# Optimization experiments

Measured on AMD Instinct MI355X. Metric: run time of the kernel, lower is better.

The kernel has to match this reference:

```python
import jax, jax.numpy as jnp
import numpy as np


def setup_inputs() -> dict:
    key = jax.random.key(0)
    ks = jax.random.split(key, 11)
    B, S, D, K = 8, 2048, 512, 256
    s = lambda k, shp, fan: jax.random.normal(k, shp, dtype=jnp.float32) / np.sqrt(fan)
    return {
        "x": jax.random.normal(ks[0], (B, S, D), dtype=jnp.float32),
        "Wk1": s(ks[1], (D, K), D), "bk1": jnp.zeros((K,), jnp.float32),
        "Wq1": s(ks[2], (D, K), D), "bq1": jnp.zeros((K,), jnp.float32),
        "Wk2": s(ks[3], (D, K), D), "bk2": jnp.zeros((K,), jnp.float32),
        "Wq2": s(ks[4], (D, K), D), "bq2": jnp.zeros((K,), jnp.float32),
        "Wv2": s(ks[5], (D, D), D), "bv2": jnp.zeros((D,), jnp.float32),
    }


def _attn(q, k, v):
    # raw scores with NO 1/sqrt(d) scaling, softmax over key axis, then AV
    scores = jax.nn.softmax(jnp.einsum('bqd,bkd->bqk', q, k), axis=-1)
    return jnp.einsum('bqk,bkd->bqd', scores, v)


def _block2(h, Wk2, bk2, Wq2, bq2, Wv2, bv2):
    k = h @ Wk2 + bk2
    q = h @ Wq2 + bq2
    v = h @ Wv2 + bv2
    v = v / jnp.linalg.norm(v, axis=2, keepdims=True)  # L2-normalize values
    return _attn(q, k, v)


def reference(x, Wk1, bk1, Wq1, bq1, Wk2, bk2, Wq2, bq2, Wv2, bv2):
    # block 1: values are the raw input x
    k1 = x @ Wk1 + bk1
    q1 = x @ Wq1 + bq1
    outputs = _attn(q1, k1, x)
    # blocks 2 and 3 reuse the SAME layer-2 weights (as in the torch forward)
    hidden = _block2(outputs, Wk2, bk2, Wq2, bq2, Wv2, bv2)
    final = _block2(hidden, Wk2, bk2, Wq2, bq2, Wv2, bv2)
    return final[0, -1, :]
```

## Files before the change

kernel.cpp:

```cpp
#include <hip/hip_runtime.h>
#include <math.h>

typedef __attribute__((ext_vector_type(8))) short short8;
typedef __attribute__((ext_vector_type(4))) float f32x4;

__device__ inline unsigned short f2bf_rn(float f) {
    unsigned u = __builtin_bit_cast(unsigned, f);
    u += 0x7FFF + ((u >> 16) & 1);
    return (unsigned short)(u >> 16);
}
__device__ inline float bf2f(unsigned short h) {
    unsigned u = ((unsigned)h) << 16;
    return __builtin_bit_cast(float, u);
}

#define ISSUE(ST, RA, RB)                                                      \
  do {                                                                         \
    int s_ = (ST);                                                             \
    int sg_ = s_ / SPS;                                                        \
    int k0_ = (s_ - sg_ * SPS) * 64;                                           \
    const unsigned short* Ap_ = (sg_ < 2) ? Ah : Al;                           \
    const unsigned short* Bp_ = (sg_ == 1) ? Bl : Bh;                          \
    _Pragma("unroll") for (int i_ = 0; i_ < 4; ++i_) {                         \
      RA[i_] = *(const uint4*)(Ap_ + (size_t)(bm + crow[i_]) * lda + k0_ + csl[i_] * 8); \
      RB[i_] = *(const uint4*)(Bp_ + (size_t)(bn + crow[i_]) * ldb + k0_ + csl[i_] * 8); \
    }                                                                          \
  } while (0)

#define PHASE(IT, RWa, RWb, RLa, RLb)                                          \
  do {                                                                         \
    _Pragma("unroll") for (int i_ = 0; i_ < 4; ++i_) {                         \
      int wsl_ = csl[i_] ^ (crow[i_] & 7);                                     \
      *(uint4*)&As[crow[i_]][wsl_ * 8] = RWa[i_];                              \
      *(uint4*)&Bs[crow[i_]][wsl_ * 8] = RWb[i_];                              \
    }                                                                          \
    if ((IT) + 1 < CHUNK) { ISSUE(st0 + (IT) + 1, RLa, RLb); }                 \
    asm volatile("s_waitcnt lgkmcnt(0)\n\ts_barrier" ::: "memory");            \
    _Pragma("unroll") for (int kk = 0; kk < 2; ++kk) {                         \
      short8 af[4], bf[4];                                                     \
      _Pragma("unroll") for (int f = 0; f < 4; ++f) {                          \
        int ar = wm * 64 + f * 16 + r15;                                       \
        int as_ = (kk * 4 + ksl) ^ (ar & 7);                                   \
        af[f] = *(const short8*)&As[ar][as_ * 8];                              \
        int br = wn * 64 + f * 16 + r15;                                       \
        int bs_ = (kk * 4 + ksl) ^ (br & 7);                                   \
        bf[f] = *(const short8*)&Bs[br][bs_ * 8];                              \
      }                                                                        \
      _Pragma("unroll") for (int i_ = 0; i_ < 4; ++i_)                         \
        _Pragma("unroll") for (int j_ = 0; j_ < 4; ++j_)                       \
          acc[i_][j_] = __builtin_amdgcn_mfma_f32_16x16x32_bf16(               \
              af[i_], bf[j_], acc[i_][j_], 0, 0, 0);                           \
    }                                                                          \
    asm volatile("s_barrier" ::: "memory");                                    \
  } while (0)

template <int KSEG, int NSPLIT>
__global__ __launch_bounds__(256, 2) void gemm_bf16(
    const unsigned short* __restrict__ Ah, const unsigned short* __restrict__ Al, int lda,
    const unsigned short* __restrict__ Bh, const unsigned short* __restrict__ Bl, int ldb,
    float* __restrict__ Cout, int ldc)
{
    constexpr int SPS = KSEG / 64;
    constexpr int NST = 3 * SPS;
    constexpr int CHUNK = NST / NSPLIT;

    __shared__ __align__(16) unsigned short As[128][64];
    __shared__ __align__(16) unsigned short Bs[128][64];

    const int tid = threadIdx.x, lane = tid & 63, w = tid >> 6;
    const int wm = w >> 1, wn = w & 1;
    const int bm = blockIdx.y * 128, bn = blockIdx.x * 128;
    const int st0 = blockIdx.z * CHUNK;
    const int r15 = lane & 15, ksl = lane >> 4;

    int crow[4], csl[4];
#pragma unroll
    for (int i = 0; i < 4; ++i) { int c = tid + i * 256; crow[i] = c >> 3; csl[i] = c & 7; }

    f32x4 acc[4][4];
#pragma unroll
    for (int i = 0; i < 4; ++i)
#pragma unroll
        for (int j = 0; j < 4; ++j) acc[i][j] = (f32x4){0.f, 0.f, 0.f, 0.f};

    uint4 rA0[4], rB0[4], rA1[4], rB1[4];
    ISSUE(st0, rA0, rB0);

#pragma unroll 1
    for (int it = 0; it < CHUNK; it += 2) {
        PHASE(it,     rA0, rB0, rA1, rB1);
        PHASE(it + 1, rA1, rB1, rA0, rB0);
    }

    float* Cz = Cout + (size_t)blockIdx.z * (size_t)(gridDim.y * 128) * ldc;
#pragma unroll
    for (int i = 0; i < 4; ++i) {
        int rowb = bm + wm * 64 + i * 16 + (lane >> 4) * 4;
#pragma unroll
        for (int j = 0; j < 4; ++j) {
            int colb = bn + wn * 64 + j * 16 + r15;
#pragma unroll
            for (int r = 0; r < 4; ++r)
                Cz[(size_t)(rowb + r) * ldc + colb] = acc[i][j][r];
        }
    }
}

template <int NS, bool BIAS>
__global__ __launch_bounds__(256) void reduce_kernel(
    const float* __restrict__ part, size_t pstride4,
    const float* __restrict__ bias, float* __restrict__ C,
    unsigned short* __restrict__ Ch, unsigned short* __restrict__ Cl, int N)
{
    size_t idx = (size_t)blockIdx.x * 256 + threadIdx.x;
    const float4* p = (const float4*)part;
    float4 s = p[idx];
#pragma unroll
    for (int z = 1; z < NS; ++z) {
        float4 t = p[idx + (size_t)z * pstride4];
        s.x += t.x; s.y += t.y; s.z += t.z; s.w += t.w;
    }
    if (BIAS) {
        int col = (int)((idx * 4) & (size_t)(N - 1));
        s.x += bias[col]; s.y += bias[col + 1]; s.z += bias[col + 2]; s.w += bias[col + 3];
    }
    ((float4*)C)[idx] = s;
    float v[4] = {s.x, s.y, s.z, s.w};
    unsigned short h[4], l[4];
#pragma unroll
    for (int q = 0; q < 4; ++q) { h[q] = f2bf_rn(v[q]); l[q] = f2bf_rn(v[q] - bf2f(h[q])); }
    uint2 hp = make_uint2((unsigned)h[0] | ((unsigned)h[1] << 16), (unsigned)h[2] | ((unsigned)h[3] << 16));
    uint2 lp = make_uint2((unsigned)l[0] | ((unsigned)l[1] << 16), (unsigned)l[2] | ((unsigned)l[3] << 16));
    ((uint2*)Ch)[idx] = hp;
    ((uint2*)Cl)[idx] = lp;
}

__global__ __launch_bounds__(256) void softmax_ph(
    const float* __restrict__ Sc, unsigned short* __restrict__ Ph,
    unsigned short* __restrict__ Pl)
{
    __shared__ float red[8];
    const int tid = threadIdx.x;
    const size_t r = blockIdx.x;
    const float4* p4 = (const float4*)(Sc + r * 2048);
    float4 a = p4[tid * 2], b = p4[tid * 2 + 1];
    float vv[8] = {a.x, a.y, a.z, a.w, b.x, b.y, b.z, b.w};

    float mx = vv[0];
#pragma unroll
    for (int i = 1; i < 8; ++i) mx = fmaxf(mx, vv[i]);
#pragma unroll
    for (int o = 32; o; o >>= 1) mx = fmaxf(mx, __shfl_down(mx, o));
    if ((tid & 63) == 0) red[tid >> 6] = mx;
    __syncthreads();
    mx = fmaxf(fmaxf(red[0], red[1]), fmaxf(red[2], red[3]));

    float e[8], sum = 0.f;
#pragma unroll
    for (int i = 0; i < 8; ++i) { e[i] = expf(vv[i] - mx); sum += e[i]; }
#pragma unroll
    for (int o = 32; o; o >>= 1) sum += __shfl_down(sum, o);
    __syncthreads();
    if ((tid & 63) == 0) red[4 + (tid >> 6)] = sum;
    __syncthreads();
    float inv = 1.f / (red[4] + red[5] + red[6] + red[7]);

    unsigned short h[8], l[8];
#pragma unroll
    for (int i = 0; i < 8; ++i) {
        float pv = e[i] * inv;
        h[i] = f2bf_rn(pv);
        l[i] = f2bf_rn(pv - bf2f(h[i]));
    }
    uint4 hp, lp;
    hp.x = (unsigned)h[0] | ((unsigned)h[1] << 16); hp.y = (unsigned)h[2] | ((unsigned)h[3] << 16);
    hp.z = (unsigned)h[4] | ((unsigned)h[5] << 16); hp.w = (unsigned)h[6] | ((unsigned)h[7] << 16);
    lp.x = (unsigned)l[0] | ((unsigned)l[1] << 16); lp.y = (unsigned)l[2] | ((unsigned)l[3] << 16);
    lp.z = (unsigned)l[4] | ((unsigned)l[5] << 16); lp.w = (unsigned)l[6] | ((unsigned)l[7] << 16);
    ((uint4*)(Ph + r * 2048))[tid] = hp;
    ((uint4*)(Pl + r * 2048))[tid] = lp;
}

__global__ __launch_bounds__(256) void l2norm_kernel(float* __restrict__ V, int ld,
                                                     int coloff, int D)
{
    __shared__ float red[8];
    const int tid = threadIdx.x;
    float* p = V + (size_t)blockIdx.x * ld + coloff;
    float s = 0.f;
    for (int i = tid; i < D; i += 256) { float v = p[i]; s = fmaf(v, v, s); }
#pragma unroll
    for (int o = 32; o; o >>= 1) s += __shfl_down(s, o);
    if ((tid & 63) == 0) red[tid >> 6] = s;
    __syncthreads();
    float scale = 1.f / sqrtf(red[0] + red[1] + red[2] + red[3]);
    for (int i = tid; i < D; i += 256) p[i] *= scale;
}

__global__ __launch_bounds__(256) void tc_kernel(
    const float* __restrict__ in, int ldin,
    unsigned short* __restrict__ oh, unsigned short* __restrict__ ol,
    int ldo, int rowoff)
{
    __shared__ float tile[32][33];
    int bx = blockIdx.x * 32, by = blockIdx.y * 32;
    int tx = threadIdx.x & 31, ty = threadIdx.x >> 5;
#pragma unroll
    for (int i = 0; i < 32; i += 8)
        tile[ty + i][tx] = in[(size_t)(by + ty + i) * ldin + bx + tx];
    __syncthreads();
#pragma unroll
    for (int i = 0; i < 32; i += 8) {
        float v = tile[tx][ty + i];
        unsigned short h = f2bf_rn(v);
        unsigned short l = f2bf_rn(v - bf2f(h));
        size_t o = (size_t)(rowoff + bx + ty + i) * ldo + by + tx;
        oh[o] = h; ol[o] = l;
    }
}

__global__ __launch_bounds__(256) void convert_hl(
    const float* __restrict__ in, unsigned short* __restrict__ oh,
    unsigned short* __restrict__ ol)
{
    size_t idx = (size_t)blockIdx.x * 256 + threadIdx.x;
    float4 s = ((const float4*)in)[idx];
    float v[4] = {s.x, s.y, s.z, s.w};
    unsigned short h[4], l[4];
#pragma unroll
    for (int q = 0; q < 4; ++q) { h[q] = f2bf_rn(v[q]); l[q] = f2bf_rn(v[q] - bf2f(h[q])); }
    uint2 hp = make_uint2((unsigned)h[0] | ((unsigned)h[1] << 16), (unsigned)h[2] | ((unsigned)h[3] << 16));
    uint2 lp = make_uint2((unsigned)l[0] | ((unsigned)l[1] << 16), (unsigned)l[2] | ((unsigned)l[3] << 16));
    ((uint2*)oh)[idx] = hp;
    ((uint2*)ol)[idx] = lp;
}

__global__ __launch_bounds__(256) void concat_bias(
    const float* bk1, const float* bq1, const float* bk2, const float* bq2,
    const float* bv2, float* b1, float* b2)
{
    int i = blockIdx.x * 256 + threadIdx.x;
    if (i < 512) b1[i] = (i < 256) ? bk1[i] : bq1[i - 256];
    if (i < 1024) b2[i] = (i < 256) ? bk2[i] : (i < 512 ? bq2[i - 256] : bv2[i - 512]);
}

template <bool HAS_BIAS>
__global__ __launch_bounds__(256) void gemv_nt(
    const float* __restrict__ a, const float* __restrict__ Bt, int ldb,
    const float* __restrict__ bias, float* __restrict__ out, int K)
{
    int w = threadIdx.x >> 6, lane = threadIdx.x & 63;
    int n = blockIdx.x * 4 + w;
    const float* row = Bt + (size_t)n * ldb;
    float s = 0.f;
    for (int k = lane; k < K; k += 64) s = fmaf(a[k], row[k], s);
#pragma unroll
    for (int o = 32; o; o >>= 1) s += __shfl_down(s, o);
    if (lane == 0) out[n] = HAS_BIAS ? s + bias[n] : s;
}

__global__ __launch_bounds__(256) void gemv_hl(
    const float* __restrict__ p, const unsigned short* __restrict__ Vh,
    const unsigned short* __restrict__ Vl, int ld, float* __restrict__ out, int K)
{
    int w = threadIdx.x >> 6, lane = threadIdx.x & 63;
    int d = blockIdx.x * 4 + w;
    const unsigned short* rh = Vh + (size_t)d * ld;
    const unsigned short* rl = Vl + (size_t)d * ld;
    float s = 0.f;
    for (int k = lane; k < K; k += 64) s = fmaf(p[k], bf2f(rh[k]) + bf2f(rl[k]), s);
#pragma unroll
    for (int o = 32; o; o >>= 1) s += __shfl_down(s, o);
    if (lane == 0) out[d] = s;
}

__global__ __launch_bounds__(256) void softmax_f32(float* __restrict__ S, int L)
{
    __shared__ float row[2048];
    __shared__ float red[8];
    const int tid = threadIdx.x;
    float* p = S + (size_t)blockIdx.x * L;
    float mx = -1e30f;
    for (int i = tid; i < L; i += 256) { float v = p[i]; row[i] = v; mx = fmaxf(mx, v); }
#pragma unroll
    for (int o = 32; o; o >>= 1) mx = fmaxf(mx, __shfl_down(mx, o));
    if ((tid & 63) == 0) red[tid >> 6] = mx;
    __syncthreads();
    mx = fmaxf(fmaxf(red[0], red[1]), fmaxf(red[2], red[3]));
    float sum = 0.f;
    for (int i = tid; i < L; i += 256) { float e = expf(row[i] - mx); row[i] = e; sum += e; }
#pragma unroll
    for (int o = 32; o; o >>= 1) sum += __shfl_down(sum, o);
    __syncthreads();
    if ((tid & 63) == 0) red[4 + (tid >> 6)] = sum;
    __syncthreads();
    float inv = 1.f / (red[4] + red[5] + red[6] + red[7]);
    for (int i = tid; i < L; i += 256) p[i] = row[i] * inv;
}

extern "C" void kernel_launch(void* const* d_in, const int* in_sizes, int n_in,
                              void* d_out, int out_size, void* d_ws, size_t ws_size,
                              hipStream_t stream)
{
    const float* x   = (const float*)d_in[0];
    const float* Wk1 = (const float*)d_in[1];
    const float* bk1 = (const float*)d_in[2];
    const float* Wq1 = (const float*)d_in[3];
    const float* bq1 = (const float*)d_in[4];
    const float* Wk2 = (const float*)d_in[5];
    const float* bk2 = (const float*)d_in[6];
    const float* Wq2 = (const float*)d_in[7];
    const float* bq2 = (const float*)d_in[8];
    const float* Wv2 = (const float*)d_in[9];
    const float* bv2 = (const float*)d_in[10];
    float* out = (float*)d_out;

    const int S = 2048, D = 512;
    typedef unsigned short us;

    char* p = (char*)d_ws;
    float* C    = (float*)p;            p += (size_t)S * 1024 * 4;
    float* SCP  = (float*)p;            p += (size_t)S * S * 4;
    float* H    = (float*)p;            p += (size_t)S * D * 4;
    us* Ph  = (us*)p; p += (size_t)S * S * 2;
    us* Pl  = (us*)p; p += (size_t)S * S * 2;
    us* Chh = (us*)p; p += (size_t)S * 1024 * 2;
    us* Cll = (us*)p; p += (size_t)S * 1024 * 2;
    us* Hh  = (us*)p; p += (size_t)S * D * 2;
    us* Hl  = (us*)p; p += (size_t)S * D * 2;
    us* xh  = (us*)p; p += (size_t)S * D * 2;
    us* xl  = (us*)p; p += (size_t)S * D * 2;
    us* VTh = (us*)p; p += (size_t)D * S * 2;
    us* VTl = (us*)p; p += (size_t)D * S * 2;
    us* WT1h = (us*)p; p += (size_t)512 * 512 * 2;
    us* WT1l = (us*)p; p += (size_t)512 * 512 * 2;
    us* WT2h = (us*)p; p += (size_t)1024 * 512 * 2;
    us* WT2l = (us*)p; p += (size_t)1024 * 512 * 2;
    float* b1 = (float*)p; p += 512 * 4;
    float* b2 = (float*)p; p += 1024 * 4;

    dim3 blk(256);
    const size_t PSTR  = (size_t)S * 512 / 4;
    const size_t PSTR2 = (size_t)S * 1024 / 4;

    convert_hl<<<dim3(S * D / 1024), blk, 0, stream>>>(x, xh, xl);
    tc_kernel<<<dim3(16, 64), blk, 0, stream>>>(x, 512, VTh, VTl, S, 0);
    tc_kernel<<<dim3(8, 16), blk, 0, stream>>>(Wk1, 256, WT1h, WT1l, 512, 0);
    tc_kernel<<<dim3(8, 16), blk, 0, stream>>>(Wq1, 256, WT1h, WT1l, 512, 256);
    tc_kernel<<<dim3(8, 16), blk, 0, stream>>>(Wk2, 256, WT2h, WT2l, 512, 0);
    tc_kernel<<<dim3(8, 16), blk, 0, stream>>>(Wq2, 256, WT2h, WT2l, 512, 256);
    tc_kernel<<<dim3(16, 16), blk, 0, stream>>>(Wv2, 512, WT2h, WT2l, 512, 512);
    concat_bias<<<dim3(4), blk, 0, stream>>>(bk1, bq1, bk2, bq2, bv2, b1, b2);

    gemm_bf16<512, 3><<<dim3(4, 16, 3), blk, 0, stream>>>(xh, xl, 512, WT1h, WT1l, 512, SCP, 512);
    reduce_kernel<3, true><<<dim3(S * 512 / 1024), blk, 0, stream>>>(SCP, PSTR, b1, C, Chh, Cll, 512);
    gemm_bf16<256, 1><<<dim3(16, 16, 1), blk, 0, stream>>>(Chh + 256, Cll + 256, 512, Chh, Cll, 512, SCP, 2048);
    softmax_ph<<<dim3(S), blk, 0, stream>>>(SCP, Ph, Pl);
    gemm_bf16<2048, 4><<<dim3(4, 16, 4), blk, 0, stream>>>(Ph, Pl, 2048, VTh, VTl, 2048, SCP, 512);
    reduce_kernel<4, false><<<dim3(S * 512 / 1024), blk, 0, stream>>>(SCP, PSTR, nullptr, H, Hh, Hl, 512);

    gemm_bf16<512, 2><<<dim3(8, 16, 2), blk, 0, stream>>>(Hh, Hl, 512, WT2h, WT2l, 512, SCP, 1024);
    reduce_kernel<2, true><<<dim3(S * 1024 / 1024), blk, 0, stream>>>(SCP, PSTR2, b2, C, Chh, Cll, 1024);
    l2norm_kernel<<<dim3(S), blk, 0, stream>>>(C, 1024, 512, 512);
    tc_kernel<<<dim3(16, 64), blk, 0, stream>>>(C + 512, 1024, VTh, VTl, S, 0);
    gemm_bf16<256, 1><<<dim3(16, 16, 1), blk, 0, stream>>>(Chh + 256, Cll + 256, 1024, Chh, Cll, 1024, SCP, 2048);
    softmax_ph<<<dim3(S), blk, 0, stream>>>(SCP, Ph, Pl);
    gemm_bf16<2048, 4><<<dim3(4, 16, 4), blk, 0, stream>>>(Ph, Pl, 2048, VTh, VTl, 2048, SCP, 512);
    reduce_kernel<4, false><<<dim3(S * 512 / 1024), blk, 0, stream>>>(SCP, PSTR, nullptr, H, Hh, Hl, 512);

    gemm_bf16<512, 2><<<dim3(8, 16, 2), blk, 0, stream>>>(Hh, Hl, 512, WT2h, WT2l, 512, SCP, 1024);
    reduce_kernel<2, true><<<dim3(S * 1024 / 1024), blk, 0, stream>>>(SCP, PSTR2, b2, C, Chh, Cll, 1024);
    l2norm_kernel<<<dim3(S), blk, 0, stream>>>(C, 1024, 512, 512);
    tc_kernel<<<dim3(16, 64), blk, 0, stream>>>(C + 512, 1024, VTh, VTl, S, 0);
    gemv_nt<false><<<dim3(S / 4), blk, 0, stream>>>(C + (size_t)(S - 1) * 1024 + 256, C, 1024, nullptr, SCP, 256);
    softmax_f32<<<dim3(1), blk, 0, stream>>>(SCP, S);
    gemv_hl<<<dim3(D / 4), blk, 0, stream>>>(SCP, VTh, VTl, S, out, S);
}
```

Before: 476.9 us.

## Replace materialized score/softmax/PV pipeline with split-K flash attention and combine

The separate QK^T GEMM, row softmax, split-K PV GEMM and reduce are replaced by a fused flash-attention kernel. Each block handles 64 queries over a 256-key slice, keeps an online max and sum, and skips rescaling when the running max grows by no more than 8. A combine kernel then merges the eight key-split partials into hi/lo bf16 outputs. This avoids writing and reading the 2048x2048 fp32 score matrix and the bf16 probability matrices. In exchange it writes 8 fp32 output partials per query and uses a heavy register footprint with many barriers per tile.

```diff
diff --git a/kernel.cpp b/kernel.cpp
--- a/kernel.cpp
+++ b/kernel.cpp
@@ -3,6 +3,7 @@
 
 typedef __attribute__((ext_vector_type(8))) short short8;
 typedef __attribute__((ext_vector_type(4))) float f32x4;
+typedef unsigned short ushort_t;
 
 __device__ inline unsigned short f2bf_rn(float f) {
     unsigned u = __builtin_bit_cast(unsigned, f);
@@ -135,50 +136,216 @@
     ((uint2*)Cl)[idx] = lp;
 }
 
-__global__ __launch_bounds__(256) void softmax_ph(
-    const float* __restrict__ Sc, unsigned short* __restrict__ Ph,
-    unsigned short* __restrict__ Pl)
-{
-    __shared__ float red[8];
+#define SLK(r, s) ((s) ^ (((s) >> 3) & 3) ^ ((((r) ^ ((r) >> 3))) & 7))
+
+__global__ __launch_bounds__(256, 2) void flash_attn(
+    const unsigned short* __restrict__ Qh, const unsigned short* __restrict__ Ql,
+    const unsigned short* __restrict__ Kh, const unsigned short* __restrict__ Kl,
+    int ldqk,
+    const unsigned short* __restrict__ VTh, const unsigned short* __restrict__ VTl,
+    float* __restrict__ Opart, float* __restrict__ Mpart, float* __restrict__ Lpart)
+{
+    const int tid = threadIdx.x, lane = tid & 63, w = tid >> 6;
+    const int z = blockIdx.x;
+    const int q0 = blockIdx.y * 64;
+    const int s0 = z * 256;
+    const int cc = lane & 15, g = lane >> 4;
+
+    __shared__ __align__(16) unsigned short KsH[32][256], KsL[32][256];
+    __shared__ __align__(16) unsigned short PsH[64][32], PsL[64][32];
+    __shared__ float Fs[64];
+    __shared__ int flagAny[4];
+
+    short8 qh[8], qlv[8];
+#pragma unroll
+    for (int ks = 0; ks < 8; ++ks) {
+        const size_t qoff = (size_t)(q0 + w * 16 + cc) * ldqk + ks * 32 + g * 8;
+        qh[ks]  = *(const short8*)(Qh + qoff);
+        qlv[ks] = *(const short8*)(Ql + qoff);
+    }
+
+    f32x4 acc[4][8];
+#pragma unroll
+    for (int a = 0; a < 4; ++a)
+#pragma unroll
+        for (int b = 0; b < 8; ++b) acc[a][b] = (f32x4){0.f, 0.f, 0.f, 0.f};
+    float m[4] = {-1e30f, -1e30f, -1e30f, -1e30f};
+    float l[4] = {0.f, 0.f, 0.f, 0.f};
+
+#pragma unroll 1
+    for (int sub = 0; sub < 8; ++sub) {
+        __syncthreads();
+#pragma unroll
+        for (int i = 0; i < 4; ++i) {
+            int idx = tid + i * 256;
+            int row = (idx >> 3) & 31;
+            int sl  = (idx & 7) | ((idx >> 8) << 3);
+            size_t go = (size_t)(s0 + sub * 32 + row) * ldqk + sl * 8;
+            uint4 vh = *(const uint4*)(Kh + go);
+            uint4 vl = *(const uint4*)(Kl + go);
+            int sw = SLK(row, sl);
+            *(uint4*)&KsH[row][sw * 8] = vh;
+            *(uint4*)&KsL[row][sw * 8] = vl;
+        }
+        __syncthreads();
+
+        f32x4 sac[2];
+        sac[0] = (f32x4){0.f, 0.f, 0.f, 0.f};
+        sac[1] = (f32x4){0.f, 0.f, 0.f, 0.f};
+#pragma unroll
+        for (int ks = 0; ks < 8; ++ks) {
+#pragma unroll
+            for (int t = 0; t < 2; ++t) {
+                int row = t * 16 + cc;
+                int sw = SLK(row, ks * 4 + g);
+                short8 bh = *(const short8*)&KsH[row][sw * 8];
+                short8 bl = *(const short8*)&KsL[row][sw * 8];
+                sac[t] = __builtin_amdgcn_mfma_f32_16x16x32_bf16(qh[ks], bh, sac[t], 0, 0, 0);
+                sac[t] = __builtin_amdgcn_mfma_f32_16x16x32_bf16(qh[ks], bl, sac[t], 0, 0, 0);
+                sac[t] = __builtin_amdgcn_mfma_f32_16x16x32_bf16(qlv[ks], bh, sac[t], 0, 0, 0);
+            }
+        }
+
+        float mt[4], fr[4];
+        bool nb = false;
+#pragma unroll
+        for (int r = 0; r < 4; ++r) {
+            float v = fmaxf(sac[0][r], sac[1][r]);
+#pragma unroll
+            for (int o = 8; o >= 1; o >>= 1) v = fmaxf(v, __shfl_xor(v, o));
+            mt[r] = v;
+            nb = nb || (v > m[r] + 8.f);
+        }
+        const int need = __any((int)nb);
+        if (need) {
+#pragma unroll
+            for (int r = 0; r < 4; ++r) {
+                float mn = fmaxf(m[r], mt[r]);
+                fr[r] = __expf(m[r] - mn);
+                m[r] = mn;
+                l[r] *= fr[r];
+            }
+        } else {
+#pragma unroll
+            for (int r = 0; r < 4; ++r) fr[r] = 1.f;
+        }
+        if (cc == 0) {
+#pragma unroll
+            for (int r = 0; r < 4; ++r) Fs[w * 16 + g * 4 + r] = fr[r];
+        }
+        if (lane == 0) flagAny[w] = need;
+
+#pragma unroll
+        for (int t = 0; t < 2; ++t) {
+            float ps[4];
+#pragma unroll
+            for (int r = 0; r < 4; ++r) {
+                float p = __expf(sac[t][r] - m[r]);
+                ps[r] = p;
+                unsigned short ph = f2bf_rn(p);
+                unsigned short pl = f2bf_rn(p - bf2f(ph));
+                int qq = w * 16 + g * 4 + r;
+                int kv = cc + 16 * t;
+                int col = (((kv >> 3) ^ (qq & 3)) << 3) | (kv & 7);
+                PsH[qq][col] = ph;
+                PsL[qq][col] = pl;
+            }
+#pragma unroll
+            for (int r = 0; r < 4; ++r) {
+                float s = ps[r];
+#pragma unroll
+                for (int o = 8; o >= 1; o >>= 1) s += __shfl_xor(s, o);
+                l[r] += s;
+            }
+        }
+        __syncthreads();
+
+        int anyf = flagAny[0] | flagAny[1] | flagAny[2] | flagAny[3];
+        if (anyf) {
+#pragma unroll
+            for (int qt = 0; qt < 4; ++qt)
+#pragma unroll
+                for (int r = 0; r < 4; ++r) {
+                    float fq = Fs[qt * 16 + g * 4 + r];
+#pragma unroll
+                    for (int dt = 0; dt < 8; ++dt) acc[qt][dt][r] *= fq;
+                }
+        }
+
+        short8 pah[4], pal[4];
+#pragma unroll
+        for (int qt = 0; qt < 4; ++qt) {
+            int qr = qt * 16 + cc;
+            int col = (g ^ (qr & 3)) << 3;
+            pah[qt] = *(const short8*)&PsH[qr][col];
+            pal[qt] = *(const short8*)&PsL[qr][col];
+        }
+#pragma unroll
+        for (int dt = 0; dt < 8; ++dt) {
+            size_t vo = (size_t)(w * 128 + dt * 16 + cc) * 2048 + s0 + sub * 32 + g * 8;
+            short8 vh = *(const short8*)(VTh + vo);
+            short8 vl = *(const short8*)(VTl + vo);
+#pragma unroll
+            for (int qt = 0; qt < 4; ++qt) {
+                acc[qt][dt] = __builtin_amdgcn_mfma_f32_16x16x32_bf16(pah[qt], vh, acc[qt][dt], 0, 0, 0);
+                acc[qt][dt] = __builtin_amdgcn_mfma_f32_16x16x32_bf16(pah[qt], vl, acc[qt][dt], 0, 0, 0);
+                acc[qt][dt] = __builtin_amdgcn_mfma_f32_16x16x32_bf16(pal[qt], vh, acc[qt][dt], 0, 0, 0);
+            }
+        }
+    }
+
+#pragma unroll
+    for (int qt = 0; qt < 4; ++qt)
+#pragma unroll
+        for (int dt = 0; dt < 8; ++dt)
+#pragma unroll
+            for (int r = 0; r < 4; ++r) {
+                int row = q0 + qt * 16 + g * 4 + r;
+                int col = w * 128 + dt * 16 + cc;
+                Opart[((size_t)z * 2048 + row) * 512 + col] = acc[qt][dt][r];
+            }
+    if (cc == 0) {
+#pragma unroll
+        for (int r = 0; r < 4; ++r) {
+            int row = q0 + w * 16 + g * 4 + r;
+            Mpart[z * 2048 + row] = m[r];
+            Lpart[z * 2048 + row] = l[r];
+        }
+    }
+}
+
+__global__ __launch_bounds__(256) void flash_combine(
+    const float* __restrict__ Opart, const float* __restrict__ Mpart,
+    const float* __restrict__ Lpart,
+    unsigned short* __restrict__ Oh, unsigned short* __restrict__ Ol)
+{
+    const int q = blockIdx.x;
     const int tid = threadIdx.x;
-    const size_t r = blockIdx.x;
-    const float4* p4 = (const float4*)(Sc + r * 2048);
-    float4 a = p4[tid * 2], b = p4[tid * 2 + 1];
-    float vv[8] = {a.x, a.y, a.z, a.w, b.x, b.y, b.z, b.w};
-
-    float mx = vv[0];
-#pragma unroll
-    for (int i = 1; i < 8; ++i) mx = fmaxf(mx, vv[i]);
-#pragma unroll
-    for (int o = 32; o; o >>= 1) mx = fmaxf(mx, __shfl_down(mx, o));
-    if ((tid & 63) == 0) red[tid >> 6] = mx;
-    __syncthreads();
-    mx = fmaxf(fmaxf(red[0], red[1]), fmaxf(red[2], red[3]));
-
-    float e[8], sum = 0.f;
-#pragma unroll
-    for (int i = 0; i < 8; ++i) { e[i] = expf(vv[i] - mx); sum += e[i]; }
-#pragma unroll
-    for (int o = 32; o; o >>= 1) sum += __shfl_down(sum, o);
-    __syncthreads();
-    if ((tid & 63) == 0) red[4 + (tid >> 6)] = sum;
-    __syncthreads();
-    float inv = 1.f / (red[4] + red[5] + red[6] + red[7]);
-
-    unsigned short h[8], l[8];
-#pragma unroll
-    for (int i = 0; i < 8; ++i) {
-        float pv = e[i] * inv;
-        h[i] = f2bf_rn(pv);
-        l[i] = f2bf_rn(pv - bf2f(h[i]));
-    }
-    uint4 hp, lp;
-    hp.x = (unsigned)h[0] | ((unsigned)h[1] << 16); hp.y = (unsigned)h[2] | ((unsigned)h[3] << 16);
-    hp.z = (unsigned)h[4] | ((unsigned)h[5] << 16); hp.w = (unsigned)h[6] | ((unsigned)h[7] << 16);
-    lp.x = (unsigned)l[0] | ((unsigned)l[1] << 16); lp.y = (unsigned)l[2] | ((unsigned)l[3] << 16);
-    lp.z = (unsigned)l[4] | ((unsigned)l[5] << 16); lp.w = (unsigned)l[6] | ((unsigned)l[7] << 16);
-    ((uint4*)(Ph + r * 2048))[tid] = hp;
-    ((uint4*)(Pl + r * 2048))[tid] = lp;
+    float wz[8];
+    float mstar = -1e30f;
+#pragma unroll
+    for (int zz = 0; zz < 8; ++zz) { wz[zz] = Mpart[zz * 2048 + q]; mstar = fmaxf(mstar, wz[zz]); }
+    float L = 0.f;
+#pragma unroll
+    for (int zz = 0; zz < 8; ++zz) {
+        float e = __expf(wz[zz] - mstar);
+        L += e * Lpart[zz * 2048 + q];
+        wz[zz] = e;
+    }
+    float invL = 1.f / L;
+    int d = tid * 2;
+    float sx = 0.f, sy = 0.f;
+#pragma unroll
+    for (int zz = 0; zz < 8; ++zz) {
+        const float2 t = *(const float2*)(Opart + ((size_t)zz * 2048 + q) * 512 + d);
+        sx += wz[zz] * t.x;
+        sy += wz[zz] * t.y;
+    }
+    sx *= invL; sy *= invL;
+    unsigned short h0 = f2bf_rn(sx), h1 = f2bf_rn(sy);
+    unsigned short l0 = f2bf_rn(sx - bf2f(h0)), l1 = f2bf_rn(sy - bf2f(h1));
+    *(unsigned*)(Oh + (size_t)q * 512 + d) = (unsigned)h0 | ((unsigned)h1 << 16);
+    *(unsigned*)(Ol + (size_t)q * 512 + d) = (unsigned)l0 | ((unsigned)l1 << 16);
 }
 
 __global__ __launch_bounds__(256) void l2norm_kernel(float* __restrict__ V, int ld,
@@ -319,11 +486,10 @@
     typedef unsigned short us;
 
     char* p = (char*)d_ws;
-    float* C    = (float*)p;            p += (size_t)S * 1024 * 4;
-    float* SCP  = (float*)p;            p += (size_t)S * S * 4;
-    float* H    = (float*)p;            p += (size_t)S * D * 4;
-    us* Ph  = (us*)p; p += (size_t)S * S * 2;
-    us* Pl  = (us*)p; p += (size_t)S * S * 2;
+    float* C   = (float*)p;  p += (size_t)S * 1024 * 4;
+    float* BIG = (float*)p;  p += (size_t)8 * S * 512 * 4;
+    float* Mp  = (float*)p;  p += (size_t)8 * S * 4;
+    float* Lp  = (float*)p;  p += (size_t)8 * S * 4;
     us* Chh = (us*)p; p += (size_t)S * 1024 * 2;
     us* Cll = (us*)p; p += (size_t)S * 1024 * 2;
     us* Hh  = (us*)p; p += (size_t)S * D * 2;
@@ -352,27 +518,26 @@
     tc_kernel<<<dim3(16, 16), blk, 0, stream>>>(Wv2, 512, WT2h, WT2l, 512, 512);
     concat_bias<<<dim3(4), blk, 0, stream>>>(bk1, bq1, bk2, bq2, bv2, b1, b2);
 
-    gemm_bf16<512, 3><<<dim3(4, 16, 3), blk, 0, stream>>>(xh, xl, 512, WT1h, WT1l, 512, SCP, 512);
-    reduce_kernel<3, true><<<dim3(S * 512 / 1024), blk, 0, stream>>>(SCP, PSTR, b1, C, Chh, Cll, 512);
-    gemm_bf16<256, 1><<<dim3(16, 16, 1), blk, 0, stream>>>(Chh + 256, Cll + 256, 512, Chh, Cll, 512, SCP, 2048);
-    softmax_ph<<<dim3(S), blk, 0, stream>>>(SCP, Ph, Pl);
-    gemm_bf16<2048, 4><<<dim3(4, 16, 4), blk, 0, stream>>>(Ph, Pl, 2048, VTh, VTl, 2048, SCP, 512);
-    reduce_kernel<4, false><<<dim3(S * 512 / 1024), blk, 0, stream>>>(SCP, PSTR, nullptr, H, Hh, Hl, 512);
-
-    gemm_bf16<512, 2><<<dim3(8, 16, 2), blk, 0, stream>>>(Hh, Hl, 512, WT2h, WT2l, 512, SCP, 1024);
-    reduce_kernel<2, true><<<dim3(S * 1024 / 1024), blk, 0, stream>>>(SCP, PSTR2, b2, C, Chh, Cll, 1024);
+    gemm_bf16<512, 3><<<dim3(4, 16, 3), blk, 0, stream>>>(xh, xl, 512, WT1h, WT1l, 512, BIG, 512);
+    reduce_kernel<3, true><<<dim3(S * 512 / 1024), blk, 0, stream>>>(BIG, PSTR, b1, C, Chh, Cll, 512);
+    flash_attn<<<dim3(8, 32), blk, 0, stream>>>(Chh + 256, Cll + 256, Chh, Cll, 512,
+                                                VTh, VTl, BIG, Mp, Lp);
+    flash_combine<<<dim3(S), blk, 0, stream>>>(BIG, Mp, Lp, Hh, Hl);
+
+    gemm_bf16<512, 2><<<dim3(8, 16, 2), blk, 0, stream>>>(Hh, Hl, 512, WT2h, WT2l, 512, BIG, 1024);
+    reduce_kernel<2, true><<<dim3(S * 1024 / 1024), blk, 0, stream>>>(BIG, PSTR2, b2, C, Chh, Cll, 1024);
     l2norm_kernel<<<dim3(S), blk, 0, stream>>>(C, 1024, 512, 512);
     tc_kernel<<<dim3(16, 64), blk, 0, stream>>>(C + 512, 1024, VTh, VTl, S, 0);
-    gemm_bf16<256, 1><<<dim3(16, 16, 1), blk, 0, stream>>>(Chh + 256, Cll + 256, 1024, Chh, Cll, 1024, SCP, 2048);
-    softmax_ph<<<dim3(S), blk, 0, stream>>>(SCP, Ph, Pl);
-    gemm_bf16<2048, 4><<<dim3(4, 16, 4), blk, 0, stream>>>(Ph, Pl, 2048, VTh, VTl, 2048, SCP, 512);
-    reduce_kernel<4, false><<<dim3(S * 512 / 1024), blk, 0, stream>>>(SCP, PSTR, nullptr, H, Hh, Hl, 512);
-
-    gemm_bf16<512, 2><<<dim3(8, 16, 2), blk, 0, stream>>>(Hh, Hl, 512, WT2h, WT2l, 512, SCP, 1024);
-    reduce_kernel<2, true><<<dim3(S * 1024 / 1024), blk, 0, stream>>>(SCP, PSTR2, b2, C, Chh, Cll, 1024);
+    flash_attn<<<dim3(8, 32), blk, 0, stream>>>(Chh + 256, Cll + 256, Chh, Cll, 1024,
+                                                VTh, VTl, BIG, Mp, Lp);
+    flash_combine<<<dim3(S), blk, 0, stream>>>(BIG, Mp, Lp, Hh, Hl);
+
+    gemm_bf16<512, 2><<<dim3(8, 16, 2), blk, 0, stream>>>(Hh, Hl, 512, WT2h, WT2l, 512, BIG, 1024);
+    reduce_kernel<2, true><<<dim3(S * 1024 / 1024), blk, 0, stream>>>(BIG, PSTR2, b2, C, Chh, Cll, 1024);
     l2norm_kernel<<<dim3(S), blk, 0, stream>>>(C, 1024, 512, 512);
     tc_kernel<<<dim3(16, 64), blk, 0, stream>>>(C + 512, 1024, VTh, VTl, S, 0);
-    gemv_nt<false><<<dim3(S / 4), blk, 0, stream>>>(C + (size_t)(S - 1) * 1024 + 256, C, 1024, nullptr, SCP, 256);
-    softmax_f32<<<dim3(1), blk, 0, stream>>>(SCP, S);
-    gemv_hl<<<dim3(D / 4), blk, 0, stream>>>(SCP, VTh, VTl, S, out, S);
-}
+    gemv_nt<false><<<dim3(S / 4), blk, 0, stream>>>(C + (size_t)(S - 1) * 1024 + 256, C, 1024,
+                                                    nullptr, BIG, 256);
+    softmax_f32<<<dim3(1), blk, 0, stream>>>(BIG, S);
+    gemv_hl<<<dim3(D / 4), blk, 0, stream>>>(BIG, VTh, VTl, S, out, S);
+}
```

Result: no change. 482.3 us (+1.1%).
